# Performance work log

Measured on AMD Instinct MI355X. Metric: run time of the kernel, lower is better.

The kernel has to match this reference:

```python
import jax, jax.numpy as jnp
import numpy as np

N_GENES = 20000
N_CELLS = 1024   # expression_dim
FM_DIM = 512     # scgpt_embed_dim
EMB = 512        # embed_dim == projection_dim
N_EDGES = 640000
EPS = 1e-5


def _layernorm(x, g, b):
    mu = jnp.mean(x, axis=-1, keepdims=True)
    var = jnp.mean((x - mu) ** 2, axis=-1, keepdims=True)
    return (x - mu) * jax.lax.rsqrt(var + EPS) * g + b


def _sage_conv(x, src, dst, Wl, bl, Wr):
    # PyG SAGEConv (mean aggr): lin_l(mean_{j in N(i)} x_j) + lin_r(x_i)
    n = x.shape[0]
    agg = jax.ops.segment_sum(x[src], dst, num_segments=n)          # [N, F]
    cnt = jax.ops.segment_sum(jnp.ones((src.shape[0],), x.dtype), dst, num_segments=n)
    mean = agg / jnp.maximum(cnt, 1.0)[:, None]
    return mean @ Wl.T + bl + x @ Wr.T


def setup_inputs() -> dict:
    key = jax.random.key(0)
    ks = jax.random.split(key, 20)
    s = 0.02
    inp = {
        'x_foundation': jax.random.normal(ks[0], (N_GENES, FM_DIM), jnp.float32),
        'x_expression': jax.random.normal(ks[1], (N_GENES, N_CELLS), jnp.float32),
        'ppi_edge_index': jax.random.randint(ks[2], (2, N_EDGES), 0, N_GENES, jnp.int32),
        # expression SAGE layer 0 (N_CELLS -> EMB)
        'Wl0': s * jax.random.normal(ks[3], (EMB, N_CELLS), jnp.float32),
        'bl0': jnp.zeros((EMB,), jnp.float32),
        'Wr0': s * jax.random.normal(ks[4], (EMB, N_CELLS), jnp.float32),
        # expression SAGE layer 1 (EMB -> EMB)
        'Wl1': s * jax.random.normal(ks[5], (EMB, EMB), jnp.float32),
        'bl1': jnp.zeros((EMB,), jnp.float32),
        'Wr1': s * jax.random.normal(ks[6], (EMB, EMB), jnp.float32),
        # foundation projection: Linear + LayerNorm
        'Wf': s * jax.random.normal(ks[7], (EMB, FM_DIM), jnp.float32),
        'bf': jnp.zeros((EMB,), jnp.float32),
        'g1': jnp.ones((EMB,), jnp.float32),
        'b1': jnp.zeros((EMB,), jnp.float32),
        # fusion layer: Linear + LayerNorm
        'Wfu': s * jax.random.normal(ks[8], (EMB, EMB), jnp.float32),
        'bfu': jnp.zeros((EMB,), jnp.float32),
        'g2': jnp.ones((EMB,), jnp.float32),
        'b2': jnp.zeros((EMB,), jnp.float32),
        # final SAGE layer (EMB -> EMB), max(1, num_layers//2) == 1 layer
        'Wl2': s * jax.random.normal(ks[9], (EMB, EMB), jnp.float32),
        'bl2': jnp.zeros((EMB,), jnp.float32),
        'Wr2': s * jax.random.normal(ks[10], (EMB, EMB), jnp.float32),
    }
    return inp


def reference(x_foundation, x_expression, ppi_edge_index,
              Wl0, bl0, Wr0, Wl1, bl1, Wr1,
              Wf, bf, g1, b1, Wfu, bfu, g2, b2,
              Wl2, bl2, Wr2):
    src, dst = ppi_edge_index[0], ppi_edge_index[1]
    # expression branch: SAGEConv -> ELU (dropout = identity in eval)
    h = jax.nn.elu(_sage_conv(x_expression, src, dst, Wl0, bl0, Wr0))
    h = jax.nn.elu(_sage_conv(h, src, dst, Wl1, bl1, Wr1))
    # foundation branch: Linear -> LayerNorm -> GELU (exact, as torch nn.GELU)
    f = jax.nn.gelu(_layernorm(x_foundation @ Wf.T + bf, g1, b1), approximate=False)
    # add fusion, then Linear -> LayerNorm -> SiLU
    fused = h + f
    fo = jax.nn.silu(_layernorm(fused @ Wfu.T + bfu, g2, b2))
    # final SAGE layer(s): SAGEConv -> ELU
    gene_emb = jax.nn.elu(_sage_conv(fo, src, dst, Wl2, bl2, Wr2))
    return gene_emb
```

## Files before the change

### kernel.cpp

```cpp
#include <hip/hip_runtime.h>
#include <hip/hip_bf16.h>
#include <math.h>

#define N_GENES 20000
#define N_CELLS 1024
#define FM_DIM  512
#define EMB     512
#define N_EDGES 640000
#define LN_EPS  1e-5f
#define SCAN_B  79
#define IDX_CAP 2560

typedef __attribute__((ext_vector_type(8))) short bf8;
typedef __attribute__((ext_vector_type(4))) float f32x4;

__device__ __forceinline__ float bflo(unsigned v) { return __uint_as_float(v << 16); }
__device__ __forceinline__ float bfhi(unsigned v) { return __uint_as_float(v & 0xffff0000u); }
__device__ __forceinline__ unsigned short f2bf(float f) {
    unsigned u = __float_as_uint(f);
    return (unsigned short)((u + 0x7fffu + ((u >> 16) & 1u)) >> 16);
}
__device__ __forceinline__ unsigned packbf(float x, float y) {
    return (unsigned)f2bf(x) | ((unsigned)f2bf(y) << 16);
}
__device__ __forceinline__ unsigned addbf2(unsigned x, unsigned y) {
    return packbf(bflo(x) + bflo(y), bfhi(x) + bfhi(y));
}
__device__ __forceinline__ uint4 pack8(float4 a, float4 b) {
    uint4 o;
    o.x = packbf(a.x, a.y);
    o.y = packbf(a.z, a.w);
    o.z = packbf(b.x, b.y);
    o.w = packbf(b.z, b.w);
    return o;
}

__device__ __forceinline__ void gload16(const unsigned short* g, unsigned short* l) {
    __builtin_amdgcn_global_load_lds(
        (const __attribute__((address_space(1))) unsigned int*)g,
        (__attribute__((address_space(3))) unsigned int*)l, 16, 0, 0);
}

__global__ __launch_bounds__(256) void k_cvtcnt(const float4* __restrict__ xe,
                                                const float4* s0, const float4* s1,
                                                const float4* s2, const float4* s3,
                                                const float4* s4, const float4* s5,
                                                const float4* s6, const float4* s7,
                                                uint4* __restrict__ Xe,
                                                uint4* __restrict__ Wb,
                                                const int* __restrict__ edst,
                                                int* __restrict__ cnt) {
    if (blockIdx.x < 2048) {
        for (int i = blockIdx.x * 256 + threadIdx.x; i < 2560000 + 327680;
             i += 2048 * 256) {
            if (i < 2560000) {
                Xe[i] = pack8(xe[2 * i], xe[2 * i + 1]);
            } else {
                int w = i - 2560000;
                const float4* src; int off;
                if (w < 65536)       { src = s0; off = w; }
                else if (w < 131072) { src = s1; off = w - 65536; }
                else if (w < 163840) { src = s2; off = w - 131072; }
                else if (w < 196608) { src = s3; off = w - 163840; }
                else if (w < 229376) { src = s4; off = w - 196608; }
                else if (w < 262144) { src = s5; off = w - 229376; }
                else if (w < 294912) { src = s6; off = w - 262144; }
                else                 { src = s7; off = w - 294912; }
                Wb[w] = pack8(src[2 * off], src[2 * off + 1]);
            }
        }
    } else {
        int e = (blockIdx.x - 2048) * 256 + threadIdx.x;
        if (e < N_EDGES) atomicAdd(&cnt[edst[e]], 1);
    }
}

__global__ __launch_bounds__(256) void k_scan1(const int* __restrict__ cnt,
                                               int* __restrict__ row_ptr,
                                               int* __restrict__ bsum) {
    __shared__ int wsum[4];
    int b = blockIdx.x, t = threadIdx.x;
    int i = b * 256 + t;
    int v = (i < N_GENES) ? cnt[i] : 0;
    int lane = t & 63, wv = t >> 6;
    int x = v;
#pragma unroll
    for (int off = 1; off < 64; off <<= 1) {
        int y = __shfl_up(x, off);
        if (lane >= off) x += y;
    }
    if (lane == 63) wsum[wv] = x;
    __syncthreads();
    if (t == 0) {
        int s = 0;
        for (int w = 0; w < 4; ++w) { int tmp = wsum[w]; wsum[w] = s; s += tmp; }
    }
    __syncthreads();
    int excl = x - v + wsum[wv];
    if (i < N_GENES) row_ptr[i] = excl;
    if (t == 255) bsum[b] = excl + v;
}

__global__ void k_scan2(const int* __restrict__ bsum, int* __restrict__ boff) {
    __shared__ int wsum[2];
    int t = threadIdx.x;
    int v = (t < SCAN_B) ? bsum[t] : 0;
    int lane = t & 63, wv = t >> 6;
    int x = v;
#pragma unroll
    for (int off = 1; off < 64; off <<= 1) {
        int y = __shfl_up(x, off);
        if (lane >= off) x += y;
    }
    if (lane == 63) wsum[wv] = x;
    __syncthreads();
    int add = (wv == 1) ? wsum[0] : 0;
    int excl = x - v + add;
    if (t < SCAN_B) boff[t] = excl;
    if (t == SCAN_B) boff[SCAN_B] = excl;
}

__global__ __launch_bounds__(256) void k_scan3(int* __restrict__ row_ptr,
                                               const int* __restrict__ boff) {
    int i = blockIdx.x * 256 + threadIdx.x;
    if (i < N_GENES) row_ptr[i] += boff[i >> 8];
    if (blockIdx.x == 0 && threadIdx.x == 0) row_ptr[N_GENES] = boff[SCAN_B];
}

__global__ __launch_bounds__(256) void k_gemm_pf(const unsigned short* __restrict__ A,
                                                 const unsigned short* __restrict__ Wl,
                                                 const unsigned short* __restrict__ Wr,
                                                 unsigned short* __restrict__ C0,
                                                 unsigned short* __restrict__ C1,
                                                 int M, int K,
                                                 const int* __restrict__ e_src,
                                                 const int* __restrict__ e_dst,
                                                 const int* __restrict__ row_ptr,
                                                 int* __restrict__ fillc,
                                                 int* __restrict__ csr) {
    __shared__ __attribute__((aligned(16))) unsigned short As[128][32];
    __shared__ __attribute__((aligned(16))) unsigned short Bs[128][32];
    if (blockIdx.y >= 160) {
        int e = ((blockIdx.y - 160) * 8 + blockIdx.x) * 256 + threadIdx.x;
        if (e < N_EDGES) {
            int d = e_dst[e];
            int slot = atomicAdd(&fillc[d], 1);
            csr[row_ptr[d] + slot] = e_src[e];
        }
        return;
    }
    int m0 = (blockIdx.x * 20 + (blockIdx.y >> 3)) * 128;
    if (m0 >= M) return;
    int sel = blockIdx.y & 7;
    const unsigned short* W = (sel < 4) ? Wl : Wr;
    unsigned short* Cp = (sel < 4) ? C0 : C1;
    int n0 = (sel & 3) * 128;
    int tid = threadIdx.x;
    int lane = tid & 63;
    int w = tid >> 6, wr = w >> 1, wc = w & 1;

    int srow = tid >> 2, sch = tid & 3;
    int rA0 = min(m0 + srow, M - 1);
    int rA1 = min(m0 + srow + 64, M - 1);
    const unsigned short* gA0 = A + (size_t)rA0 * K + sch * 8;
    const unsigned short* gA1 = A + (size_t)rA1 * K + sch * 8;
    const unsigned short* gB0 = W + (size_t)(n0 + srow) * K + sch * 8;
    const unsigned short* gB1 = W + (size_t)(n0 + srow + 64) * K + sch * 8;
    unsigned short* lA0 = &As[0][0] + tid * 8;
    unsigned short* lA1 = &As[64][0] + tid * 8;
    unsigned short* lB0 = &Bs[0][0] + tid * 8;
    unsigned short* lB1 = &Bs[64][0] + tid * 8;

    f32x4 acc[4][4];
#pragma unroll
    for (int i = 0; i < 4; ++i)
#pragma unroll
        for (int j = 0; j < 4; ++j) acc[i][j] = (f32x4){0.f, 0.f, 0.f, 0.f};

    for (int k0 = 0; k0 < K; k0 += 32) {
        __syncthreads();
        gload16(gA0 + k0, lA0);
        gload16(gA1 + k0, lA1);
        gload16(gB0 + k0, lB0);
        gload16(gB1 + k0, lB1);
        __syncthreads();
        bf8 af[4], bff[4];
#pragma unroll
        for (int f = 0; f < 4; ++f) {
            af[f]  = *(const bf8*)&As[wr * 64 + f * 16 + (lane & 15)][(lane >> 4) * 8];
            bff[f] = *(const bf8*)&Bs[wc * 64 + f * 16 + (lane & 15)][(lane >> 4) * 8];
        }
#pragma unroll
        for (int i = 0; i < 4; ++i)
#pragma unroll
            for (int j = 0; j < 4; ++j)
                acc[i][j] = __builtin_amdgcn_mfma_f32_16x16x32_bf16(af[i], bff[j],
                                                                    acc[i][j], 0, 0, 0);
    }

#pragma unroll
    for (int i = 0; i < 4; ++i) {
        int rb = m0 + wr * 64 + i * 16 + (lane >> 4) * 4;
#pragma unroll
        for (int j = 0; j < 4; ++j) {
            int cc = n0 + wc * 64 + j * 16 + (lane & 15);
#pragma unroll
            for (int e = 0; e < 4; ++e) {
                int r = rb + e;
                if (r < M) Cp[(size_t)r * EMB + cc] = f2bf(acc[i][j][e]);
            }
        }
    }
}

__global__ __launch_bounds__(256) void k_gemm_fu(const unsigned short* __restrict__ A,
                                                 const unsigned short* __restrict__ A2,
                                                 const unsigned short* __restrict__ W,
                                                 unsigned short* __restrict__ Cp,
                                                 int M, int K) {
    __shared__ __attribute__((aligned(16))) unsigned short As[128][32];
    __shared__ __attribute__((aligned(16))) unsigned short Bs[128][32];
    int m0 = (blockIdx.x * 20 + (blockIdx.y >> 2)) * 128;
    if (m0 >= M) return;
    int n0 = (blockIdx.y & 3) * 128;
    int tid = threadIdx.x;
    int lane = tid & 63;
    int w = tid >> 6, wr = w >> 1, wc = w & 1;

    int srow = tid >> 2, sch = tid & 3;
    int rA0 = min(m0 + srow, M - 1);
    int rA1 = min(m0 + srow + 64, M - 1);
    const unsigned short* gA0 = A + (size_t)rA0 * K + sch * 8;
    const unsigned short* gA1 = A + (size_t)rA1 * K + sch * 8;
    const unsigned short* hA0 = A2 + (size_t)rA0 * K + sch * 8;
    const unsigned short* hA1 = A2 + (size_t)rA1 * K + sch * 8;
    const unsigned short* gB0 = W + (size_t)(n0 + srow) * K + sch * 8;
    const unsigned short* gB1 = W + (size_t)(n0 + srow + 64) * K + sch * 8;
    unsigned short* lA0 = &As[0][0] + tid * 8;
    unsigned short* lA1 = &As[64][0] + tid * 8;
    unsigned short* lB0 = &Bs[0][0] + tid * 8;
    unsigned short* lB1 = &Bs[64][0] + tid * 8;

    f32x4 acc[4][4];
#pragma unroll
    for (int i = 0; i < 4; ++i)
#pragma unroll
        for (int j = 0; j < 4; ++j) acc[i][j] = (f32x4){0.f, 0.f, 0.f, 0.f};

    for (int k0 = 0; k0 < K; k0 += 32) {
        uint4 x0 = *(const uint4*)(gA0 + k0);
        uint4 y0 = *(const uint4*)(hA0 + k0);
        uint4 x1 = *(const uint4*)(gA1 + k0);
        uint4 y1 = *(const uint4*)(hA1 + k0);
        uint4 a0, a1;
        a0.x = addbf2(x0.x, y0.x); a0.y = addbf2(x0.y, y0.y);
        a0.z = addbf2(x0.z, y0.z); a0.w = addbf2(x0.w, y0.w);
        a1.x = addbf2(x1.x, y1.x); a1.y = addbf2(x1.y, y1.y);
        a1.z = addbf2(x1.z, y1.z); a1.w = addbf2(x1.w, y1.w);
        __syncthreads();
        *(uint4*)lA0 = a0;
        *(uint4*)lA1 = a1;
        gload16(gB0 + k0, lB0);
        gload16(gB1 + k0, lB1);
        __syncthreads();
        bf8 af[4], bff[4];
#pragma unroll
        for (int f = 0; f < 4; ++f) {
            af[f]  = *(const bf8*)&As[wr * 64 + f * 16 + (lane & 15)][(lane >> 4) * 8];
            bff[f] = *(const bf8*)&Bs[wc * 64 + f * 16 + (lane & 15)][(lane >> 4) * 8];
        }
#pragma unroll
        for (int i = 0; i < 4; ++i)
#pragma unroll
            for (int j = 0; j < 4; ++j)
                acc[i][j] = __builtin_amdgcn_mfma_f32_16x16x32_bf16(af[i], bff[j],
                                                                    acc[i][j], 0, 0, 0);
    }

#pragma unroll
    for (int i = 0; i < 4; ++i) {
        int rb = m0 + wr * 64 + i * 16 + (lane >> 4) * 4;
#pragma unroll
        for (int j = 0; j < 4; ++j) {
            int cc = n0 + wc * 64 + j * 16 + (lane & 15);
#pragma unroll
            for (int e = 0; e < 4; ++e) {
                int r = rb + e;
                if (r < M) Cp[(size_t)r * EMB + cc] = f2bf(acc[i][j][e]);
            }
        }
    }
}

__global__ __launch_bounds__(256) void k_gemm_p(const unsigned short* __restrict__ A,
                                                const unsigned short* __restrict__ Wl,
                                                const unsigned short* __restrict__ Wr,
                                                unsigned short* __restrict__ C0,
                                                unsigned short* __restrict__ C1,
                                                int M, int K) {
    __shared__ __attribute__((aligned(16))) unsigned short As[128][32];
    __shared__ __attribute__((aligned(16))) unsigned short Bs[128][32];
    int m0 = (blockIdx.x * 20 + (blockIdx.y >> 3)) * 128;
    if (m0 >= M) return;
    int sel = blockIdx.y & 7;
    const unsigned short* W = (sel < 4) ? Wl : Wr;
    unsigned short* Cp = (sel < 4) ? C0 : C1;
    int n0 = (sel & 3) * 128;
    int tid = threadIdx.x;
    int lane = tid & 63;
    int w = tid >> 6, wr = w >> 1, wc = w & 1;

    int srow = tid >> 2, sch = tid & 3;
    int rA0 = min(m0 + srow, M - 1);
    int rA1 = min(m0 + srow + 64, M - 1);
    const unsigned short* gA0 = A + (size_t)rA0 * K + sch * 8;
    const unsigned short* gA1 = A + (size_t)rA1 * K + sch * 8;
    const unsigned short* gB0 = W + (size_t)(n0 + srow) * K + sch * 8;
    const unsigned short* gB1 = W + (size_t)(n0 + srow + 64) * K + sch * 8;
    unsigned short* lA0 = &As[0][0] + tid * 8;
    unsigned short* lA1 = &As[64][0] + tid * 8;
    unsigned short* lB0 = &Bs[0][0] + tid * 8;
    unsigned short* lB1 = &Bs[64][0] + tid * 8;

    f32x4 acc[4][4];
#pragma unroll
    for (int i = 0; i < 4; ++i)
#pragma unroll
        for (int j = 0; j < 4; ++j) acc[i][j] = (f32x4){0.f, 0.f, 0.f, 0.f};

    for (int k0 = 0; k0 < K; k0 += 32) {
        __syncthreads();
        gload16(gA0 + k0, lA0);
        gload16(gA1 + k0, lA1);
        gload16(gB0 + k0, lB0);
        gload16(gB1 + k0, lB1);
        __syncthreads();
        bf8 af[4], bff[4];
#pragma unroll
        for (int f = 0; f < 4; ++f) {
            af[f]  = *(const bf8*)&As[wr * 64 + f * 16 + (lane & 15)][(lane >> 4) * 8];
            bff[f] = *(const bf8*)&Bs[wc * 64 + f * 16 + (lane & 15)][(lane >> 4) * 8];
        }
#pragma unroll
        for (int i = 0; i < 4; ++i)
#pragma unroll
            for (int j = 0; j < 4; ++j)
                acc[i][j] = __builtin_amdgcn_mfma_f32_16x16x32_bf16(af[i], bff[j],
                                                                    acc[i][j], 0, 0, 0);
    }

#pragma unroll
    for (int i = 0; i < 4; ++i) {
        int rb = m0 + wr * 64 + i * 16 + (lane >> 4) * 4;
#pragma unroll
        for (int j = 0; j < 4; ++j) {
            int cc = n0 + wc * 64 + j * 16 + (lane & 15);
#pragma unroll
            for (int e = 0; e < 4; ++e) {
                int r = rb + e;
                if (r < M) Cp[(size_t)r * EMB + cc] = f2bf(acc[i][j][e]);
            }
        }
    }
}

__global__ __launch_bounds__(256) void k_gemm_3(const unsigned short* __restrict__ A1,
                                                const float* __restrict__ A2,
                                                const unsigned short* __restrict__ Wl,
                                                const unsigned short* __restrict__ Wr,
                                                const unsigned short* __restrict__ Wf,
                                                unsigned short* __restrict__ C0,
                                                unsigned short* __restrict__ C1,
                                                unsigned short* __restrict__ CF,
                                                int M) {
    const int K = 512;
    __shared__ __attribute__((aligned(16))) unsigned short As[128][32];
    __shared__ __attribute__((aligned(16))) unsigned short Bs[128][32];
    int y = blockIdx.y;
    bool fpath = (y >= 160);
    int m0, n0;
    const unsigned short* W;
    unsigned short* Cp;
    if (!fpath) {
        m0 = (blockIdx.x * 20 + (y >> 3)) * 128;
        int sel = y & 7;
        W = (sel < 4) ? Wl : Wr;
        Cp = (sel < 4) ? C0 : C1;
        n0 = (sel & 3) * 128;
    } else {
        int y2 = y - 160;
        m0 = (blockIdx.x * 20 + (y2 >> 2)) * 128;
        n0 = (y2 & 3) * 128;
        W = Wf;
        Cp = CF;
    }
    if (m0 >= M) return;
    int tid = threadIdx.x;
    int lane = tid & 63;
    int w = tid >> 6, wr = w >> 1, wc = w & 1;

    int srow = tid >> 2, sch = tid & 3;
    int rA0 = min(m0 + srow, M - 1);
    int rA1 = min(m0 + srow + 64, M - 1);
    const unsigned short* gA0 = A1 + (size_t)rA0 * K + sch * 8;
    const unsigned short* gA1 = A1 + (size_t)rA1 * K + sch * 8;
    const float* fA0 = A2 + (size_t)rA0 * K + sch * 8;
    const float* fA1 = A2 + (size_t)rA1 * K + sch * 8;
    const unsigned short* gB0 = W + (size_t)(n0 + srow) * K + sch * 8;
    const unsigned short* gB1 = W + (size_t)(n0 + srow + 64) * K + sch * 8;
    unsigned short* lA0 = &As[0][0] + tid * 8;
    unsigned short* lA1 = &As[64][0] + tid * 8;
    unsigned short* lB0 = &Bs[0][0] + tid * 8;
    unsigned short* lB1 = &Bs[64][0] + tid * 8;

    f32x4 acc[4][4];
#pragma unroll
    for (int i = 0; i < 4; ++i)
#pragma unroll
        for (int j = 0; j < 4; ++j) acc[i][j] = (f32x4){0.f, 0.f, 0.f, 0.f};

    for (int k0 = 0; k0 < K; k0 += 32) {
        uint4 a0, a1;
        if (fpath) {
            a0 = pack8(*(const float4*)(fA0 + k0), *(const float4*)(fA0 + k0 + 4));
            a1 = pack8(*(const float4*)(fA1 + k0), *(const float4*)(fA1 + k0 + 4));
        }
        __syncthreads();
        if (fpath) {
            *(uint4*)lA0 = a0;
            *(uint4*)lA1 = a1;
        } else {
            gload16(gA0 + k0, lA0);
            gload16(gA1 + k0, lA1);
        }
        gload16(gB0 + k0, lB0);
        gload16(gB1 + k0, lB1);
        __syncthreads();
        bf8 af[4], bff[4];
#pragma unroll
        for (int f = 0; f < 4; ++f) {
            af[f]  = *(const bf8*)&As[wr * 64 + f * 16 + (lane & 15)][(lane >> 4) * 8];
            bff[f] = *(const bf8*)&Bs[wc * 64 + f * 16 + (lane & 15)][(lane >> 4) * 8];
        }
#pragma unroll
        for (int i = 0; i < 4; ++i)
#pragma unroll
            for (int j = 0; j < 4; ++j)
                acc[i][j] = __builtin_amdgcn_mfma_f32_16x16x32_bf16(af[i], bff[j],
                                                                    acc[i][j], 0, 0, 0);
    }

#pragma unroll
    for (int i = 0; i < 4; ++i) {
        int rb = m0 + wr * 64 + i * 16 + (lane >> 4) * 4;
#pragma unroll
        for (int j = 0; j < 4; ++j) {
            int cc = n0 + wc * 64 + j * 16 + (lane & 15);
#pragma unroll
            for (int e = 0; e < 4; ++e) {
                int r = rb + e;
                if (r < M) Cp[(size_t)r * EMB + cc] = f2bf(acc[i][j][e]);
            }
        }
    }
}

template <int OUTF32>
__device__ __forceinline__ void sage_body(const unsigned short* yl,
                                          const unsigned short* yr,
                                          const float* bl,
                                          const int* row_ptr,
                                          const int* csr,
                                          void* outp, int slice, int nblk,
                                          int* sIdx) {
    int g = threadIdx.x >> 3;
    int l = threadIdx.x & 7;
    int node = nblk * 32 + g;
    int w = slice * 8 + l;
    int s32 = row_ptr[nblk * 32];
    int e32 = row_ptr[nblk * 32 + 32];
    int nIdx = e32 - s32;
    bool lds_ok = (nIdx <= IDX_CAP);
    if (lds_ok) {
        for (int i = threadIdx.x; i < nIdx; i += 256) sIdx[i] = csr[s32 + i];
    }
    __syncthreads();
    int s = row_ptr[node], e = row_ptr[node + 1];
    int deg = e - s;
    const char* Yb = (const char*)yl;
    unsigned lb = (unsigned)(w << 4);
    float ac[8];
#pragma unroll
    for (int q = 0; q < 8; ++q) ac[q] = 0.f;
    if (lds_ok) {
        int lp = s - s32;
        int p = 0;
        for (; p + 8 <= deg; p += 8) {
            int j[8];
#pragma unroll
            for (int q = 0; q < 8; ++q) j[q] = sIdx[lp + p + q];
            uint4 v[8];
#pragma unroll
            for (int q = 0; q < 8; ++q)
// ... 115 lines not shown

__global__ __launch_bounds__(256) void k_sageln(const unsigned short* __restrict__ C0,
                                                const unsigned short* __restrict__ C1,
                                                const float* __restrict__ bl1,
                                                const int* __restrict__ row_ptr,
                                                const int* __restrict__ csr,
                                                unsigned short* __restrict__ Pd,
                                                const unsigned short* __restrict__ F0,
                                                const float* __restrict__ bf_,
                                                const float* __restrict__ g1,
                                                const float* __restrict__ b1,
                                                unsigned short* __restrict__ fout) {
    __shared__ int sIdx[IDX_CAP];
    if (blockIdx.y < 625) {
        sage_body<0>(C0, C1, bl1, row_ptr, csr, Pd, blockIdx.x, blockIdx.y, sIdx);
    } else {
        ln_body<0>(F0, bf_, g1, b1, fout, (blockIdx.y - 625) * 8 + blockIdx.x);
    }
}

extern "C" void kernel_launch(void* const* d_in, const int* in_sizes, int n_in,
                              void* d_out, int out_size, void* d_ws, size_t ws_size,
                              hipStream_t stream) {
    const float* x_found = (const float*)d_in[0];
    const float* x_exp   = (const float*)d_in[1];
    const int*   ppi     = (const int*)d_in[2];
    const float* Wl0 = (const float*)d_in[3];
    const float* bl0 = (const float*)d_in[4];
    const float* Wr0 = (const float*)d_in[5];
    const float* Wl1 = (const float*)d_in[6];
    const float* bl1 = (const float*)d_in[7];
    const float* Wr1 = (const float*)d_in[8];
    const float* Wf  = (const float*)d_in[9];
    const float* bf_ = (const float*)d_in[10];
    const float* g1  = (const float*)d_in[11];
    const float* b1  = (const float*)d_in[12];
    const float* Wfu = (const float*)d_in[13];
    const float* bfu = (const float*)d_in[14];
    const float* g2  = (const float*)d_in[15];
    const float* b2  = (const float*)d_in[16];
    const float* Wl2 = (const float*)d_in[17];
    const float* bl2 = (const float*)d_in[18];
    const float* Wr2 = (const float*)d_in[19];

    const int* e_src = ppi;
    const int* e_dst = ppi + N_EDGES;

    char* ws = (char*)d_ws;
    unsigned short* C0   = (unsigned short*)(ws);
    unsigned short* C1   = (unsigned short*)(ws + 20480000);
    unsigned short* actA = (unsigned short*)(ws + 40960000);
    int* cnt     = (int*)(ws + 61440000);
    int* row_ptr = (int*)(ws + 61520000);
    int* fillc   = (int*)(ws + 61600064);
    int* csr     = (int*)(ws + 61680064);
    unsigned short* Wb = (unsigned short*)(ws + 64240064);
    unsigned short* Wl0b = Wb;
    unsigned short* Wr0b = Wb + 524288;
    unsigned short* Wl1b = Wb + 1048576;
    unsigned short* Wr1b = Wb + 1310720;
    unsigned short* Wfb  = Wb + 1572864;
    unsigned short* Wfub = Wb + 1835008;
    unsigned short* Wl2b = Wb + 2097152;
    unsigned short* Wr2b = Wb + 2359296;
    int* bsum = (int*)(ws + 69482944);
    int* boff = (int*)(ws + 69483264);

    unsigned short* Xe = (unsigned short*)d_out;
    unsigned short* Pd = (unsigned short*)d_out;
    unsigned short* F0 = (unsigned short*)d_out + 10240000;

    hipMemsetAsync(cnt, 0, N_GENES * sizeof(int), stream);
    hipMemsetAsync(fillc, 0, N_GENES * sizeof(int), stream);
    k_cvtcnt<<<4548, 256, 0, stream>>>((const float4*)x_exp,
                                       (const float4*)Wl0, (const float4*)Wr0,
                                       (const float4*)Wl1, (const float4*)Wr1,
                                       (const float4*)Wf,  (const float4*)Wfu,
                                       (const float4*)Wl2, (const float4*)Wr2,
                                       (uint4*)Xe, (uint4*)Wb, e_dst, cnt);
    k_scan1<<<SCAN_B, 256, 0, stream>>>(cnt, row_ptr, bsum);
    k_scan2<<<1, 128, 0, stream>>>(bsum, boff);
    k_scan3<<<SCAN_B, 256, 0, stream>>>(row_ptr, boff);

    dim3 gg(8, 80);
    dim3 gp(8, 160);
    dim3 g3(8, 240);
    dim3 gpf(8, 473);
    dim3 gs(8, 625);
    dim3 gsl(8, 3125);

    k_gemm_pf<<<gpf, 256, 0, stream>>>(Xe, Wl0b, Wr0b, C0, C1, N_GENES, N_CELLS,
                                       e_src, e_dst, row_ptr, fillc, csr);
    k_sage_b<0><<<gs, 256, 0, stream>>>(C0, C1, bl0, row_ptr, csr, actA);

    k_gemm_3<<<g3, 256, 0, stream>>>(actA, x_found, Wl1b, Wr1b, Wfb,
                                     C0, C1, F0, N_GENES);
    k_sageln<<<gsl, 256, 0, stream>>>(C0, C1, bl1, row_ptr, csr,
                                      Pd, F0, bf_, g1, b1, actA);

    k_gemm_fu<<<gg, 256, 0, stream>>>(Pd, actA, Wfub, C0, N_GENES, EMB);
    k_ln_b<1><<<N_GENES, 256, 0, stream>>>(C0, bfu, g2, b2, actA);

    k_gemm_p<<<gp, 256, 0, stream>>>(actA, Wl2b, Wr2b, C0, C1, N_GENES, EMB);
    k_sage_b<1><<<gs, 256, 0, stream>>>(C0, C1, bl2, row_ptr, csr, (float*)d_out);
}
```

Baseline: 432.3 us.

## Double-buffer LDS tiles in all GEMM kernels to overlap loads with MFMA

Each of the four bf16 MFMA GEMM kernels now uses two shared-memory tile buffers. The next K-slice is staged while the current slice is computed, which cuts the per-iteration barriers from two to one. The register-staged A paths (bf16 add and fp32-to-bf16 pack) also prefetch the next slice into registers one step ahead. This doubles LDS use per block and raises register pressure, which may reduce occupancy.

```diff
diff --git a/kernel.cpp b/kernel.cpp
--- a/kernel.cpp
+++ b/kernel.cpp
@@ -138,8 +138,8 @@
                                                  const int* __restrict__ row_ptr,
                                                  int* __restrict__ fillc,
                                                  int* __restrict__ csr) {
-    __shared__ __attribute__((aligned(16))) unsigned short As[128][32];
-    __shared__ __attribute__((aligned(16))) unsigned short Bs[128][32];
+    __shared__ __attribute__((aligned(16))) unsigned short As[2][128][32];
+    __shared__ __attribute__((aligned(16))) unsigned short Bs[2][128][32];
     if (blockIdx.y >= 160) {
         int e = ((blockIdx.y - 160) * 8 + blockIdx.x) * 256 + threadIdx.x;
         if (e < N_EDGES) {
@@ -166,10 +166,6 @@
     const unsigned short* gA1 = A + (size_t)rA1 * K + sch * 8;
     const unsigned short* gB0 = W + (size_t)(n0 + srow) * K + sch * 8;
     const unsigned short* gB1 = W + (size_t)(n0 + srow + 64) * K + sch * 8;
-    unsigned short* lA0 = &As[0][0] + tid * 8;
-    unsigned short* lA1 = &As[64][0] + tid * 8;
-    unsigned short* lB0 = &Bs[0][0] + tid * 8;
-    unsigned short* lB1 = &Bs[64][0] + tid * 8;
 
     f32x4 acc[4][4];
 #pragma unroll
@@ -177,18 +173,22 @@
 #pragma unroll
         for (int j = 0; j < 4; ++j) acc[i][j] = (f32x4){0.f, 0.f, 0.f, 0.f};
 
-    for (int k0 = 0; k0 < K; k0 += 32) {
-        __syncthreads();
-        gload16(gA0 + k0, lA0);
-        gload16(gA1 + k0, lA1);
-        gload16(gB0 + k0, lB0);
-        gload16(gB1 + k0, lB1);
-        __syncthreads();
+    auto stage = [&](int b, int k0) {
+        unsigned short* Ab = &As[0][0][0] + b * (128 * 32);
+        unsigned short* Bb = &Bs[0][0][0] + b * (128 * 32);
+        gload16(gA0 + k0, Ab + tid * 8);
+        gload16(gA1 + k0, Ab + 64 * 32 + tid * 8);
+        gload16(gB0 + k0, Bb + tid * 8);
+        gload16(gB1 + k0, Bb + 64 * 32 + tid * 8);
+    };
+    auto compute = [&](int b) {
+        const unsigned short* Ab = &As[0][0][0] + b * (128 * 32);
+        const unsigned short* Bb = &Bs[0][0][0] + b * (128 * 32);
         bf8 af[4], bff[4];
 #pragma unroll
         for (int f = 0; f < 4; ++f) {
-            af[f]  = *(const bf8*)&As[wr * 64 + f * 16 + (lane & 15)][(lane >> 4) * 8];
-            bff[f] = *(const bf8*)&Bs[wc * 64 + f * 16 + (lane & 15)][(lane >> 4) * 8];
+            af[f]  = *(const bf8*)(Ab + (wr * 64 + f * 16 + (lane & 15)) * 32 + (lane >> 4) * 8);
+            bff[f] = *(const bf8*)(Bb + (wc * 64 + f * 16 + (lane & 15)) * 32 + (lane >> 4) * 8);
         }
 #pragma unroll
         for (int i = 0; i < 4; ++i)
@@ -196,7 +196,18 @@
             for (int j = 0; j < 4; ++j)
                 acc[i][j] = __builtin_amdgcn_mfma_f32_16x16x32_bf16(af[i], bff[j],
                                                                     acc[i][j], 0, 0, 0);
-    }
+    };
+
+    stage(0, 0);
+    __syncthreads();
+    int cur = 0;
+    for (int k0 = 32; k0 < K; k0 += 32) {
+        stage(cur ^ 1, k0);
+        compute(cur);
+        __syncthreads();
+        cur ^= 1;
+    }
+    compute(cur);
 
 #pragma unroll
     for (int i = 0; i < 4; ++i) {
@@ -218,8 +229,8 @@
                                                  const unsigned short* __restrict__ W,
                                                  unsigned short* __restrict__ Cp,
                                                  int M, int K) {
-    __shared__ __attribute__((aligned(16))) unsigned short As[128][32];
-    __shared__ __attribute__((aligned(16))) unsigned short Bs[128][32];
+    __shared__ __attribute__((aligned(16))) unsigned short As[2][128][32];
+    __shared__ __attribute__((aligned(16))) unsigned short Bs[2][128][32];
     int m0 = (blockIdx.x * 20 + (blockIdx.y >> 2)) * 128;
     if (m0 >= M) return;
     int n0 = (blockIdx.y & 3) * 128;
@@ -236,10 +247,6 @@
     const unsigned short* hA1 = A2 + (size_t)rA1 * K + sch * 8;
     const unsigned short* gB0 = W + (size_t)(n0 + srow) * K + sch * 8;
     const unsigned short* gB1 = W + (size_t)(n0 + srow + 64) * K + sch * 8;
-    unsigned short* lA0 = &As[0][0] + tid * 8;
-    unsigned short* lA1 = &As[64][0] + tid * 8;
-    unsigned short* lB0 = &Bs[0][0] + tid * 8;
-    unsigned short* lB1 = &Bs[64][0] + tid * 8;
 
     f32x4 acc[4][4];
 #pragma unroll
@@ -247,27 +254,36 @@
 #pragma unroll
         for (int j = 0; j < 4; ++j) acc[i][j] = (f32x4){0.f, 0.f, 0.f, 0.f};
 
-    for (int k0 = 0; k0 < K; k0 += 32) {
-        uint4 x0 = *(const uint4*)(gA0 + k0);
-        uint4 y0 = *(const uint4*)(hA0 + k0);
-        uint4 x1 = *(const uint4*)(gA1 + k0);
-        uint4 y1 = *(const uint4*)(hA1 + k0);
+    uint4 nx0, ny0, nx1, ny1;
+    auto loadA = [&](int k0) {
+        nx0 = *(const uint4*)(gA0 + k0);
+        ny0 = *(const uint4*)(hA0 + k0);
+        nx1 = *(const uint4*)(gA1 + k0);
+        ny1 = *(const uint4*)(hA1 + k0);
+    };
+    auto stageA = [&](int b) {
         uint4 a0, a1;
-        a0.x = addbf2(x0.x, y0.x); a0.y = addbf2(x0.y, y0.y);
-        a0.z = addbf2(x0.z, y0.z); a0.w = addbf2(x0.w, y0.w);
-        a1.x = addbf2(x1.x, y1.x); a1.y = addbf2(x1.y, y1.y);
-        a1.z = addbf2(x1.z, y1.z); a1.w = addbf2(x1.w, y1.w);
-        __syncthreads();
-        *(uint4*)lA0 = a0;
-        *(uint4*)lA1 = a1;
-        gload16(gB0 + k0, lB0);
-        gload16(gB1 + k0, lB1);
-        __syncthreads();
+        a0.x = addbf2(nx0.x, ny0.x); a0.y = addbf2(nx0.y, ny0.y);
+        a0.z = addbf2(nx0.z, ny0.z); a0.w = addbf2(nx0.w, ny0.w);
+        a1.x = addbf2(nx1.x, ny1.x); a1.y = addbf2(nx1.y, ny1.y);
+        a1.z = addbf2(nx1.z, ny1.z); a1.w = addbf2(nx1.w, ny1.w);
+        unsigned short* Ab = &As[0][0][0] + b * (128 * 32);
+        *(uint4*)(Ab + tid * 8) = a0;
+        *(uint4*)(Ab + 64 * 32 + tid * 8) = a1;
+    };
+    auto stageB = [&](int b, int k0) {
+        unsigned short* Bb = &Bs[0][0][0] + b * (128 * 32);
+        gload16(gB0 + k0, Bb + tid * 8);
+        gload16(gB1 + k0, Bb + 64 * 32 + tid * 8);
+    };
+    auto compute = [&](int b) {
+        const unsigned short* Ab = &As[0][0][0] + b * (128 * 32);
+        const unsigned short* Bb = &Bs[0][0][0] + b * (128 * 32);
         bf8 af[4], bff[4];
 #pragma unroll
         for (int f = 0; f < 4; ++f) {
-            af[f]  = *(const bf8*)&As[wr * 64 + f * 16 + (lane & 15)][(lane >> 4) * 8];
-            bff[f] = *(const bf8*)&Bs[wc * 64 + f * 16 + (lane & 15)][(lane >> 4) * 8];
+            af[f]  = *(const bf8*)(Ab + (wr * 64 + f * 16 + (lane & 15)) * 32 + (lane >> 4) * 8);
+            bff[f] = *(const bf8*)(Bb + (wc * 64 + f * 16 + (lane & 15)) * 32 + (lane >> 4) * 8);
         }
 #pragma unroll
         for (int i = 0; i < 4; ++i)
@@ -275,7 +291,25 @@
             for (int j = 0; j < 4; ++j)
                 acc[i][j] = __builtin_amdgcn_mfma_f32_16x16x32_bf16(af[i], bff[j],
                                                                     acc[i][j], 0, 0, 0);
-    }
+    };
+
+    const int NT = K / 32;
+    loadA(0);
+    stageA(0);
+    stageB(0, 0);
+    loadA(32);
+    __syncthreads();
+    int cur = 0;
+    for (int t = 1; t < NT; ++t) {
+        int k0 = t * 32;
+        stageA(cur ^ 1);
+        if (t + 1 < NT) loadA(k0 + 32);
+        stageB(cur ^ 1, k0);
+        compute(cur);
+        __syncthreads();
+        cur ^= 1;
+    }
+    compute(cur);
 
 #pragma unroll
     for (int i = 0; i < 4; ++i) {
@@ -298,8 +332,8 @@
                                                 unsigned short* __restrict__ C0,
                                                 unsigned short* __restrict__ C1,
                                                 int M, int K) {
-    __shared__ __attribute__((aligned(16))) unsigned short As[128][32];
-    __shared__ __attribute__((aligned(16))) unsigned short Bs[128][32];
+    __shared__ __attribute__((aligned(16))) unsigned short As[2][128][32];
+    __shared__ __attribute__((aligned(16))) unsigned short Bs[2][128][32];
     int m0 = (blockIdx.x * 20 + (blockIdx.y >> 3)) * 128;
     if (m0 >= M) return;
     int sel = blockIdx.y & 7;
@@ -317,10 +351,6 @@
     const unsigned short* gA1 = A + (size_t)rA1 * K + sch * 8;
     const unsigned short* gB0 = W + (size_t)(n0 + srow) * K + sch * 8;
     const unsigned short* gB1 = W + (size_t)(n0 + srow + 64) * K + sch * 8;
-    unsigned short* lA0 = &As[0][0] + tid * 8;
-    unsigned short* lA1 = &As[64][0] + tid * 8;
-    unsigned short* lB0 = &Bs[0][0] + tid * 8;
-    unsigned short* lB1 = &Bs[64][0] + tid * 8;
 
     f32x4 acc[4][4];
 #pragma unroll
@@ -328,18 +358,22 @@
 #pragma unroll
         for (int j = 0; j < 4; ++j) acc[i][j] = (f32x4){0.f, 0.f, 0.f, 0.f};
 
-    for (int k0 = 0; k0 < K; k0 += 32) {
-        __syncthreads();
-        gload16(gA0 + k0, lA0);
-        gload16(gA1 + k0, lA1);
-        gload16(gB0 + k0, lB0);
-        gload16(gB1 + k0, lB1);
-        __syncthreads();
+    auto stage = [&](int b, int k0) {
+        unsigned short* Ab = &As[0][0][0] + b * (128 * 32);
+        unsigned short* Bb = &Bs[0][0][0] + b * (128 * 32);
+        gload16(gA0 + k0, Ab + tid * 8);
+        gload16(gA1 + k0, Ab + 64 * 32 + tid * 8);
+        gload16(gB0 + k0, Bb + tid * 8);
+        gload16(gB1 + k0, Bb + 64 * 32 + tid * 8);
+    };
+    auto compute = [&](int b) {
+        const unsigned short* Ab = &As[0][0][0] + b * (128 * 32);
+        const unsigned short* Bb = &Bs[0][0][0] + b * (128 * 32);
         bf8 af[4], bff[4];
 #pragma unroll
         for (int f = 0; f < 4; ++f) {
-            af[f]  = *(const bf8*)&As[wr * 64 + f * 16 + (lane & 15)][(lane >> 4) * 8];
-            bff[f] = *(const bf8*)&Bs[wc * 64 + f * 16 + (lane & 15)][(lane >> 4) * 8];
+            af[f]  = *(const bf8*)(Ab + (wr * 64 + f * 16 + (lane & 15)) * 32 + (lane >> 4) * 8);
+            bff[f] = *(const bf8*)(Bb + (wc * 64 + f * 16 + (lane & 15)) * 32 + (lane >> 4) * 8);
         }
 #pragma unroll
         for (int i = 0; i < 4; ++i)
@@ -347,7 +381,18 @@
             for (int j = 0; j < 4; ++j)
                 acc[i][j] = __builtin_amdgcn_mfma_f32_16x16x32_bf16(af[i], bff[j],
                                                                     acc[i][j], 0, 0, 0);
-    }
+    };
+
+    stage(0, 0);
+    __syncthreads();
+    int cur = 0;
+    for (int k0 = 32; k0 < K; k0 += 32) {
+        stage(cur ^ 1, k0);
+        compute(cur);
+        __syncthreads();
+        cur ^= 1;
+    }
+    compute(cur);
 
 #pragma unroll
     for (int i = 0; i < 4; ++i) {
@@ -374,8 +419,8 @@
                                                 unsigned short* __restrict__ CF,
                                                 int M) {
     const int K = 512;
-    __shared__ __attribute__((aligned(16))) unsigned short As[128][32];
-    __shared__ __attribute__((aligned(16))) unsigned short Bs[128][32];
+    __shared__ __attribute__((aligned(16))) unsigned short As[2][128][32];
+    __shared__ __attribute__((aligned(16))) unsigned short Bs[2][128][32];
     int y = blockIdx.y;
     bool fpath = (y >= 160);
     int m0, n0;
@@ -408,10 +453,6 @@
     const float* fA1 = A2 + (size_t)rA1 * K + sch * 8;
     const unsigned short* gB0 = W + (size_t)(n0 + srow) * K + sch * 8;
     const unsigned short* gB1 = W + (size_t)(n0 + srow + 64) * K + sch * 8;
-    unsigned short* lA0 = &As[0][0] + tid * 8;
-    unsigned short* lA1 = &As[64][0] + tid * 8;
-    unsigned short* lB0 = &Bs[0][0] + tid * 8;
-    unsigned short* lB1 = &Bs[64][0] + tid * 8;
 
     f32x4 acc[4][4];
 #pragma unroll
@@ -419,28 +460,36 @@
 #pragma unroll
         for (int j = 0; j < 4; ++j) acc[i][j] = (f32x4){0.f, 0.f, 0.f, 0.f};
 
-    for (int k0 = 0; k0 < K; k0 += 32) {
-        uint4 a0, a1;
-        if (fpath) {
-            a0 = pack8(*(const float4*)(fA0 + k0), *(const float4*)(fA0 + k0 + 4));
-            a1 = pack8(*(const float4*)(fA1 + k0), *(const float4*)(fA1 + k0 + 4));
-        }
-        __syncthreads();
-        if (fpath) {
-            *(uint4*)lA0 = a0;
-            *(uint4*)lA1 = a1;
-        } else {
-            gload16(gA0 + k0, lA0);
-            gload16(gA1 + k0, lA1);
-        }
-        gload16(gB0 + k0, lB0);
-        gload16(gB1 + k0, lB1);
-        __syncthreads();
+    float4 n0a, n0b, n1a, n1b;
+    auto loadF = [&](int k0) {
+        n0a = *(const float4*)(fA0 + k0);
+        n0b = *(const float4*)(fA0 + k0 + 4);
+        n1a = *(const float4*)(fA1 + k0);
+        n1b = *(const float4*)(fA1 + k0 + 4);
+    };
+    auto stageAf = [&](int b) {
+        unsigned short* Ab = &As[0][0][0] + b * (128 * 32);
+        *(uint4*)(Ab + tid * 8) = pack8(n0a, n0b);
+        *(uint4*)(Ab + 64 * 32 + tid * 8) = pack8(n1a, n1b);
+    };
+    auto stageAb = [&](int b, int k0) {
+        unsigned short* Ab = &As[0][0][0] + b * (128 * 32);
+        gload16(gA0 + k0, Ab + tid * 8);
+        gload16(gA1 + k0, Ab + 64 * 32 + tid * 8);
+    };
+    auto stageB = [&](int b, int k0) {
+        unsigned short* Bb = &Bs[0][0][0] + b * (128 * 32);
+        gload16(gB0 + k0, Bb + tid * 8);
+        gload16(gB1 + k0, Bb + 64 * 32 + tid * 8);
+    };
+    auto compute = [&](int b) {
+        const unsigned short* Ab = &As[0][0][0] + b * (128 * 32);
+        const unsigned short* Bb = &Bs[0][0][0] + b * (128 * 32);
         bf8 af[4], bff[4];
 #pragma unroll
         for (int f = 0; f < 4; ++f) {
-            af[f]  = *(const bf8*)&As[wr * 64 + f * 16 + (lane & 15)][(lane >> 4) * 8];
-            bff[f] = *(const bf8*)&Bs[wc * 64 + f * 16 + (lane & 15)][(lane >> 4) * 8];
+            af[f]  = *(const bf8*)(Ab + (wr * 64 + f * 16 + (lane & 15)) * 32 + (lane >> 4) * 8);
+            bff[f] = *(const bf8*)(Bb + (wc * 64 + f * 16 + (lane & 15)) * 32 + (lane >> 4) * 8);
         }
 #pragma unroll
         for (int i = 0; i < 4; ++i)
@@ -448,7 +497,33 @@
             for (int j = 0; j < 4; ++j)
                 acc[i][j] = __builtin_amdgcn_mfma_f32_16x16x32_bf16(af[i], bff[j],
                                                                     acc[i][j], 0, 0, 0);
-    }
+    };
+
+    const int NT = K / 32;
+    if (fpath) {
+        loadF(0);
+        stageAf(0);
+        loadF(32);
+    } else {
+        stageAb(0, 0);
+    }
+    stageB(0, 0);
+    __syncthreads();
+    int cur = 0;
+    for (int t = 1; t < NT; ++t) {
+        int k0 = t * 32;
+        if (fpath) {
+            stageAf(cur ^ 1);
+            if (t + 1 < NT) loadF(k0 + 32);
+        } else {
+            stageAb(cur ^ 1, k0);
+        }
+        stageB(cur ^ 1, k0);
+        compute(cur);
+        __syncthreads();
+        cur ^= 1;
+    }
+    compute(cur);
 
 #pragma unroll
     for (int i = 0; i < 4; ++i) {
```

Result: slower. 466.7 us (+8.0%).

## Double-buffer LDS in SAGE GEMM and XOR-swizzle LDS tiles in all GEMMs

Applied to the files above, without the earlier changes.

The first SAGE GEMM now uses two LDS buffers, so the global-to-LDS copy of the next K tile is issued while MFMAs run on the current one, and it needs one barrier per tile instead of two. Every GEMM kernel also applies an XOR swizzle to the 16-byte chunk index, both in the global source address and in the fragment reads, to cut LDS bank conflicts. The double buffer doubles LDS use per block, which may lower occupancy, and the loop assumes K/32 is even.

```diff
diff --git a/kernel.cpp b/kernel.cpp
--- a/kernel.cpp
+++ b/kernel.cpp
@@ -40,6 +40,7 @@
         (const __attribute__((address_space(1))) unsigned int*)g,
         (__attribute__((address_space(3))) unsigned int*)l, 16, 0, 0);
 }
+
 
 __global__ __launch_bounds__(256) void k_cvtcnt(const float4* __restrict__ xe,
                                                 const float4* s0, const float4* s1,
@@ -138,8 +139,8 @@
                                                  const int* __restrict__ row_ptr,
                                                  int* __restrict__ fillc,
                                                  int* __restrict__ csr) {
-    __shared__ __attribute__((aligned(16))) unsigned short As[128][32];
-    __shared__ __attribute__((aligned(16))) unsigned short Bs[128][32];
+    __shared__ __attribute__((aligned(16))) unsigned short As[2][128][32];
+    __shared__ __attribute__((aligned(16))) unsigned short Bs[2][128][32];
     if (blockIdx.y >= 160) {
         int e = ((blockIdx.y - 160) * 8 + blockIdx.x) * 256 + threadIdx.x;
         if (e < N_EDGES) {
@@ -160,16 +161,14 @@
     int w = tid >> 6, wr = w >> 1, wc = w & 1;
 
     int srow = tid >> 2, sch = tid & 3;
+    int schs = (sch ^ (srow & 3));
     int rA0 = min(m0 + srow, M - 1);
     int rA1 = min(m0 + srow + 64, M - 1);
-    const unsigned short* gA0 = A + (size_t)rA0 * K + sch * 8;
-    const unsigned short* gA1 = A + (size_t)rA1 * K + sch * 8;
-    const unsigned short* gB0 = W + (size_t)(n0 + srow) * K + sch * 8;
-    const unsigned short* gB1 = W + (size_t)(n0 + srow + 64) * K + sch * 8;
-    unsigned short* lA0 = &As[0][0] + tid * 8;
-    unsigned short* lA1 = &As[64][0] + tid * 8;
-    unsigned short* lB0 = &Bs[0][0] + tid * 8;
-    unsigned short* lB1 = &Bs[64][0] + tid * 8;
+    const unsigned short* gA0 = A + (size_t)rA0 * K + schs * 8;
+    const unsigned short* gA1 = A + (size_t)rA1 * K + schs * 8;
+    const unsigned short* gB0 = W + (size_t)(n0 + srow) * K + schs * 8;
+    const unsigned short* gB1 = W + (size_t)(n0 + srow + 64) * K + schs * 8;
+    int rswz = ((lane >> 4) ^ (lane & 3)) * 8;
 
     f32x4 acc[4][4];
 #pragma unroll
@@ -177,18 +176,22 @@
 #pragma unroll
         for (int j = 0; j < 4; ++j) acc[i][j] = (f32x4){0.f, 0.f, 0.f, 0.f};
 
-    for (int k0 = 0; k0 < K; k0 += 32) {
-        __syncthreads();
-        gload16(gA0 + k0, lA0);
-        gload16(gA1 + k0, lA1);
-        gload16(gB0 + k0, lB0);
-        gload16(gB1 + k0, lB1);
-        __syncthreads();
+    auto stage = [&](int b, int k0) {
+        unsigned short* Ab = &As[b][0][0];
+        unsigned short* Bb = &Bs[b][0][0];
+        gload16(gA0 + k0, Ab + tid * 8);
+        gload16(gA1 + k0, Ab + 64 * 32 + tid * 8);
+        gload16(gB0 + k0, Bb + tid * 8);
+        gload16(gB1 + k0, Bb + 64 * 32 + tid * 8);
+    };
+    auto compute = [&](int b) {
+        const unsigned short* Ab = &As[b][0][0];
+        const unsigned short* Bb = &Bs[b][0][0];
         bf8 af[4], bff[4];
 #pragma unroll
         for (int f = 0; f < 4; ++f) {
-            af[f]  = *(const bf8*)&As[wr * 64 + f * 16 + (lane & 15)][(lane >> 4) * 8];
-            bff[f] = *(const bf8*)&Bs[wc * 64 + f * 16 + (lane & 15)][(lane >> 4) * 8];
+            af[f]  = *(const bf8*)(Ab + (wr * 64 + f * 16 + (lane & 15)) * 32 + rswz);
+            bff[f] = *(const bf8*)(Bb + (wc * 64 + f * 16 + (lane & 15)) * 32 + rswz);
         }
 #pragma unroll
         for (int i = 0; i < 4; ++i)
@@ -196,6 +199,18 @@
             for (int j = 0; j < 4; ++j)
                 acc[i][j] = __builtin_amdgcn_mfma_f32_16x16x32_bf16(af[i], bff[j],
                                                                     acc[i][j], 0, 0, 0);
+    };
+
+    const int NT = K / 32;
+    stage(0, 0);
+    __syncthreads();
+    for (int t = 0; t < NT; t += 2) {
+        stage(1, (t + 1) * 32);
+        compute(0);
+        __syncthreads();
+        if (t + 2 < NT) stage(0, (t + 2) * 32);
+        compute(1);
+        __syncthreads();
     }
 
 #pragma unroll
@@ -228,18 +243,20 @@
     int w = tid >> 6, wr = w >> 1, wc = w & 1;
 
     int srow = tid >> 2, sch = tid & 3;
+    int schs = (sch ^ (srow & 3));
     int rA0 = min(m0 + srow, M - 1);
     int rA1 = min(m0 + srow + 64, M - 1);
-    const unsigned short* gA0 = A + (size_t)rA0 * K + sch * 8;
-    const unsigned short* gA1 = A + (size_t)rA1 * K + sch * 8;
-    const unsigned short* hA0 = A2 + (size_t)rA0 * K + sch * 8;
-    const unsigned short* hA1 = A2 + (size_t)rA1 * K + sch * 8;
-    const unsigned short* gB0 = W + (size_t)(n0 + srow) * K + sch * 8;
-    const unsigned short* gB1 = W + (size_t)(n0 + srow + 64) * K + sch * 8;
+    const unsigned short* gA0 = A + (size_t)rA0 * K + schs * 8;
+    const unsigned short* gA1 = A + (size_t)rA1 * K + schs * 8;
+    const unsigned short* hA0 = A2 + (size_t)rA0 * K + schs * 8;
+    const unsigned short* hA1 = A2 + (size_t)rA1 * K + schs * 8;
+    const unsigned short* gB0 = W + (size_t)(n0 + srow) * K + schs * 8;
+    const unsigned short* gB1 = W + (size_t)(n0 + srow + 64) * K + schs * 8;
     unsigned short* lA0 = &As[0][0] + tid * 8;
     unsigned short* lA1 = &As[64][0] + tid * 8;
     unsigned short* lB0 = &Bs[0][0] + tid * 8;
     unsigned short* lB1 = &Bs[64][0] + tid * 8;
+    int rswz = ((lane >> 4) ^ (lane & 3)) * 8;
 
     f32x4 acc[4][4];
 #pragma unroll
@@ -266,8 +283,8 @@
         bf8 af[4], bff[4];
 #pragma unroll
         for (int f = 0; f < 4; ++f) {
-            af[f]  = *(const bf8*)&As[wr * 64 + f * 16 + (lane & 15)][(lane >> 4) * 8];
-            bff[f] = *(const bf8*)&Bs[wc * 64 + f * 16 + (lane & 15)][(lane >> 4) * 8];
+            af[f]  = *(const bf8*)(&As[0][0] + (wr * 64 + f * 16 + (lane & 15)) * 32 + rswz);
+            bff[f] = *(const bf8*)(&Bs[0][0] + (wc * 64 + f * 16 + (lane & 15)) * 32 + rswz);
         }
 #pragma unroll
         for (int i = 0; i < 4; ++i)
@@ -311,16 +328,18 @@
     int w = tid >> 6, wr = w >> 1, wc = w & 1;
 
     int srow = tid >> 2, sch = tid & 3;
+    int schs = (sch ^ (srow & 3));
     int rA0 = min(m0 + srow, M - 1);
     int rA1 = min(m0 + srow + 64, M - 1);
-    const unsigned short* gA0 = A + (size_t)rA0 * K + sch * 8;
-    const unsigned short* gA1 = A + (size_t)rA1 * K + sch * 8;
-    const unsigned short* gB0 = W + (size_t)(n0 + srow) * K + sch * 8;
-    const unsigned short* gB1 = W + (size_t)(n0 + srow + 64) * K + sch * 8;
+    const unsigned short* gA0 = A + (size_t)rA0 * K + schs * 8;
+    const unsigned short* gA1 = A + (size_t)rA1 * K + schs * 8;
+    const unsigned short* gB0 = W + (size_t)(n0 + srow) * K + schs * 8;
+    const unsigned short* gB1 = W + (size_t)(n0 + srow + 64) * K + schs * 8;
     unsigned short* lA0 = &As[0][0] + tid * 8;
     unsigned short* lA1 = &As[64][0] + tid * 8;
     unsigned short* lB0 = &Bs[0][0] + tid * 8;
     unsigned short* lB1 = &Bs[64][0] + tid * 8;
+    int rswz = ((lane >> 4) ^ (lane & 3)) * 8;
 
     f32x4 acc[4][4];
 #pragma unroll
@@ -338,8 +357,8 @@
         bf8 af[4], bff[4];
 #pragma unroll
         for (int f = 0; f < 4; ++f) {
-            af[f]  = *(const bf8*)&As[wr * 64 + f * 16 + (lane & 15)][(lane >> 4) * 8];
-            bff[f] = *(const bf8*)&Bs[wc * 64 + f * 16 + (lane & 15)][(lane >> 4) * 8];
+            af[f]  = *(const bf8*)(&As[0][0] + (wr * 64 + f * 16 + (lane & 15)) * 32 + rswz);
+            bff[f] = *(const bf8*)(&Bs[0][0] + (wc * 64 + f * 16 + (lane & 15)) * 32 + rswz);
         }
 #pragma unroll
         for (int i = 0; i < 4; ++i)
@@ -400,18 +419,20 @@
     int w = tid >> 6, wr = w >> 1, wc = w & 1;
 
     int srow = tid >> 2, sch = tid & 3;
+    int schs = (sch ^ (srow & 3));
     int rA0 = min(m0 + srow, M - 1);
     int rA1 = min(m0 + srow + 64, M - 1);
-    const unsigned short* gA0 = A1 + (size_t)rA0 * K + sch * 8;
-    const unsigned short* gA1 = A1 + (size_t)rA1 * K + sch * 8;
-    const float* fA0 = A2 + (size_t)rA0 * K + sch * 8;
-    const float* fA1 = A2 + (size_t)rA1 * K + sch * 8;
-    const unsigned short* gB0 = W + (size_t)(n0 + srow) * K + sch * 8;
-    const unsigned short* gB1 = W + (size_t)(n0 + srow + 64) * K + sch * 8;
+    const unsigned short* gA0 = A1 + (size_t)rA0 * K + schs * 8;
+    const unsigned short* gA1 = A1 + (size_t)rA1 * K + schs * 8;
+    const float* fA0 = A2 + (size_t)rA0 * K + schs * 8;
+    const float* fA1 = A2 + (size_t)rA1 * K + schs * 8;
+    const unsigned short* gB0 = W + (size_t)(n0 + srow) * K + schs * 8;
+    const unsigned short* gB1 = W + (size_t)(n0 + srow + 64) * K + schs * 8;
     unsigned short* lA0 = &As[0][0] + tid * 8;
     unsigned short* lA1 = &As[64][0] + tid * 8;
     unsigned short* lB0 = &Bs[0][0] + tid * 8;
     unsigned short* lB1 = &Bs[64][0] + tid * 8;
+    int rswz = ((lane >> 4) ^ (lane & 3)) * 8;
 
     f32x4 acc[4][4];
 #pragma unroll
@@ -439,8 +460,8 @@
         bf8 af[4], bff[4];
 #pragma unroll
         for (int f = 0; f < 4; ++f) {
-            af[f]  = *(const bf8*)&As[wr * 64 + f * 16 + (lane & 15)][(lane >> 4) * 8];
-            bff[f] = *(const bf8*)&Bs[wc * 64 + f * 16 + (lane & 15)][(lane >> 4) * 8];
+            af[f]  = *(const bf8*)(&As[0][0] + (wr * 64 + f * 16 + (lane & 15)) * 32 + rswz);
+            bff[f] = *(const bf8*)(&Bs[0][0] + (wc * 64 + f * 16 + (lane & 15)) * 32 + rswz);
         }
 #pragma unroll
         for (int i = 0; i < 4; ++i)
```

Result: no change. 435.9 us (+0.8%).

## Double-buffer LDS in layer-0 GEMM and record edge slots during count

Applied to the files above, without the earlier changes.

The layer-0 GEMM now keeps two LDS buffers, so the global-to-LDS load of the next K tile is issued before the MFMA work on the current tile, with one barrier per tile instead of two. CSR fill no longer runs a second atomic pass: the count kernel keeps each edge's atomicAdd return value as a byte slot, and the fill phase writes directly to row_ptr+slot. This drops a memset and 640k atomics at the cost of a byte array and doubled LDS. The byte slot silently wraps if any node has more than 255 incoming edges.

```diff
diff --git a/kernel.cpp b/kernel.cpp
--- a/kernel.cpp
+++ b/kernel.cpp
@@ -49,7 +49,8 @@
                                                 uint4* __restrict__ Xe,
                                                 uint4* __restrict__ Wb,
                                                 const int* __restrict__ edst,
-                                                int* __restrict__ cnt) {
+                                                int* __restrict__ cnt,
+                                                unsigned char* __restrict__ eslot) {
     if (blockIdx.x < 2048) {
         for (int i = blockIdx.x * 256 + threadIdx.x; i < 2560000 + 327680;
              i += 2048 * 256) {
@@ -71,7 +72,10 @@
         }
     } else {
         int e = (blockIdx.x - 2048) * 256 + threadIdx.x;
-        if (e < N_EDGES) atomicAdd(&cnt[edst[e]], 1);
+        if (e < N_EDGES) {
+            int old = atomicAdd(&cnt[edst[e]], 1);
+            eslot[e] = (unsigned char)old;
+        }
     }
 }
 
@@ -136,16 +140,15 @@
                                                  const int* __restrict__ e_src,
                                                  const int* __restrict__ e_dst,
                                                  const int* __restrict__ row_ptr,
-                                                 int* __restrict__ fillc,
+                                                 const unsigned char* __restrict__ eslot,
                                                  int* __restrict__ csr) {
-    __shared__ __attribute__((aligned(16))) unsigned short As[128][32];
-    __shared__ __attribute__((aligned(16))) unsigned short Bs[128][32];
+    __shared__ __attribute__((aligned(16))) unsigned short As[2][128][32];
+    __shared__ __attribute__((aligned(16))) unsigned short Bs[2][128][32];
     if (blockIdx.y >= 160) {
         int e = ((blockIdx.y - 160) * 8 + blockIdx.x) * 256 + threadIdx.x;
         if (e < N_EDGES) {
             int d = e_dst[e];
-            int slot = atomicAdd(&fillc[d], 1);
-            csr[row_ptr[d] + slot] = e_src[e];
+            csr[row_ptr[d] + (int)eslot[e]] = e_src[e];
         }
         return;
     }
@@ -166,10 +169,6 @@
     const unsigned short* gA1 = A + (size_t)rA1 * K + sch * 8;
     const unsigned short* gB0 = W + (size_t)(n0 + srow) * K + sch * 8;
     const unsigned short* gB1 = W + (size_t)(n0 + srow + 64) * K + sch * 8;
-    unsigned short* lA0 = &As[0][0] + tid * 8;
-    unsigned short* lA1 = &As[64][0] + tid * 8;
-    unsigned short* lB0 = &Bs[0][0] + tid * 8;
-    unsigned short* lB1 = &Bs[64][0] + tid * 8;
 
     f32x4 acc[4][4];
 #pragma unroll
@@ -177,18 +176,22 @@
 #pragma unroll
         for (int j = 0; j < 4; ++j) acc[i][j] = (f32x4){0.f, 0.f, 0.f, 0.f};
 
-    for (int k0 = 0; k0 < K; k0 += 32) {
-        __syncthreads();
-        gload16(gA0 + k0, lA0);
-        gload16(gA1 + k0, lA1);
-        gload16(gB0 + k0, lB0);
-        gload16(gB1 + k0, lB1);
-        __syncthreads();
+    auto stage = [&](int b, int k0) {
+        unsigned short* Ab = &As[b][0][0];
+        unsigned short* Bb = &Bs[b][0][0];
+        gload16(gA0 + k0, Ab + tid * 8);
+        gload16(gA1 + k0, Ab + 64 * 32 + tid * 8);
+        gload16(gB0 + k0, Bb + tid * 8);
+        gload16(gB1 + k0, Bb + 64 * 32 + tid * 8);
+    };
+    auto compute = [&](int b) {
+        const unsigned short* Ab = &As[b][0][0];
+        const unsigned short* Bb = &Bs[b][0][0];
         bf8 af[4], bff[4];
 #pragma unroll
         for (int f = 0; f < 4; ++f) {
-            af[f]  = *(const bf8*)&As[wr * 64 + f * 16 + (lane & 15)][(lane >> 4) * 8];
-            bff[f] = *(const bf8*)&Bs[wc * 64 + f * 16 + (lane & 15)][(lane >> 4) * 8];
+            af[f]  = *(const bf8*)(Ab + (wr * 64 + f * 16 + (lane & 15)) * 32 + (lane >> 4) * 8);
+            bff[f] = *(const bf8*)(Bb + (wc * 64 + f * 16 + (lane & 15)) * 32 + (lane >> 4) * 8);
         }
 #pragma unroll
         for (int i = 0; i < 4; ++i)
@@ -196,6 +199,18 @@
             for (int j = 0; j < 4; ++j)
                 acc[i][j] = __builtin_amdgcn_mfma_f32_16x16x32_bf16(af[i], bff[j],
                                                                     acc[i][j], 0, 0, 0);
+    };
+
+    const int NT = K / 32;
+    stage(0, 0);
+    __syncthreads();
+    for (int t = 0; t < NT; t += 2) {
+        stage(1, (t + 1) * 32);
+        compute(0);
+        __syncthreads();
+        if (t + 2 < NT) stage(0, (t + 2) * 32);
+        compute(1);
+        __syncthreads();
     }
 
 #pragma unroll
@@ -670,9 +685,9 @@
     unsigned short* actA = (unsigned short*)(ws + 40960000);
     int* cnt     = (int*)(ws + 61440000);
     int* row_ptr = (int*)(ws + 61520000);
-    int* fillc   = (int*)(ws + 61600064);
-    int* csr     = (int*)(ws + 61680064);
-    unsigned short* Wb = (unsigned short*)(ws + 64240064);
+    unsigned char* eslot = (unsigned char*)(ws + 61600064);
+    int* csr     = (int*)(ws + 62240064);
+    unsigned short* Wb = (unsigned short*)(ws + 64800064);
     unsigned short* Wl0b = Wb;
     unsigned short* Wr0b = Wb + 524288;
     unsigned short* Wl1b = Wb + 1048576;
@@ -681,21 +696,20 @@
     unsigned short* Wfub = Wb + 1835008;
     unsigned short* Wl2b = Wb + 2097152;
     unsigned short* Wr2b = Wb + 2359296;
-    int* bsum = (int*)(ws + 69482944);
-    int* boff = (int*)(ws + 69483264);
+    int* bsum = (int*)(ws + 70042944);
+    int* boff = (int*)(ws + 70043264);
 
     unsigned short* Xe = (unsigned short*)d_out;
     unsigned short* Pd = (unsigned short*)d_out;
     unsigned short* F0 = (unsigned short*)d_out + 10240000;
 
     hipMemsetAsync(cnt, 0, N_GENES * sizeof(int), stream);
-    hipMemsetAsync(fillc, 0, N_GENES * sizeof(int), stream);
     k_cvtcnt<<<4548, 256, 0, stream>>>((const float4*)x_exp,
                                        (const float4*)Wl0, (const float4*)Wr0,
                                        (const float4*)Wl1, (const float4*)Wr1,
                                        (const float4*)Wf,  (const float4*)Wfu,
                                        (const float4*)Wl2, (const float4*)Wr2,
-                                       (uint4*)Xe, (uint4*)Wb, e_dst, cnt);
+                                       (uint4*)Xe, (uint4*)Wb, e_dst, cnt, eslot);
     k_scan1<<<SCAN_B, 256, 0, stream>>>(cnt, row_ptr, bsum);
     k_scan2<<<1, 128, 0, stream>>>(bsum, boff);
     k_scan3<<<SCAN_B, 256, 0, stream>>>(row_ptr, boff);
@@ -708,7 +722,7 @@
     dim3 gsl(8, 3125);
 
     k_gemm_pf<<<gpf, 256, 0, stream>>>(Xe, Wl0b, Wr0b, C0, C1, N_GENES, N_CELLS,
-                                       e_src, e_dst, row_ptr, fillc, csr);
+                                       e_src, e_dst, row_ptr, eslot, csr);
     k_sage_b<0><<<gs, 256, 0, stream>>>(C0, C1, bl0, row_ptr, csr, actA);
 
     k_gemm_3<<<g3, 256, 0, stream>>>(actA, x_found, Wl1b, Wr1b, Wfb,
```

After: 417.2 us. -3.5%, faster.
